# Optimization experiments

Measured on AMD Instinct MI355X. Metric: run time of the kernel, lower is better.

The kernel has to match this reference:

```python
import jax, jax.numpy as jnp
import numpy as np

IN_FEATURES = 512
OUT_FEATURES = 512
GRID_SIZE = 8
SPLINE_ORDER = 3


def make_grid():
    # grid has grid_size + 2*spline_order + 1 knots in [-1, 1]
    return jnp.linspace(-1.0, 1.0, GRID_SIZE + 2 * SPLINE_ORDER + 1, dtype=jnp.float32)


def b_splines(x, grid):
    # x: (N, in)  ->  bases: (N, in, grid_size + spline_order)
    x = jnp.clip(x, -2.0, 2.0)[..., None]  # (N, in, 1)
    bases = ((x >= grid[:-1]) & (x < grid[1:])).astype(x.dtype)
    for k in range(1, SPLINE_ORDER + 1):
        denom1 = grid[k:-1] - grid[:-(k + 1)]
        denom1 = jnp.where(jnp.abs(denom1) < 1e-8, jnp.ones_like(denom1), denom1)
        denom2 = grid[k + 1:] - grid[1:-k]
        denom2 = jnp.where(jnp.abs(denom2) < 1e-8, jnp.ones_like(denom2), denom2)
        bases = ((x - grid[:-(k + 1)]) / denom1 * bases[..., :-1]
                 + (grid[k + 1:] - x) / denom2 * bases[..., 1:])
    return bases


def setup_inputs() -> dict:
    key = jax.random.key(0)
    kx, kb, ks = jax.random.split(key, 3)
    x = jax.random.normal(kx, (8192, IN_FEATURES), dtype=jnp.float32)
    # xavier_uniform with gain=0.5 for base_weight
    limit = 0.5 * np.sqrt(6.0 / (IN_FEATURES + OUT_FEATURES))
    base_weight = jax.random.uniform(kb, (OUT_FEATURES, IN_FEATURES), dtype=jnp.float32,
                                     minval=-limit, maxval=limit)
    spline_weight = 0.01 * jax.random.normal(
        ks, (OUT_FEATURES, IN_FEATURES, GRID_SIZE + SPLINE_ORDER), dtype=jnp.float32)
    return {"x": x, "base_weight": base_weight, "spline_weight": spline_weight}


def reference(x, base_weight, spline_weight):
    grid = make_grid()
    base_out = x @ base_weight.T                      # (N, out)
    basis = b_splines(x, grid)                        # (N, in, G+K)
    spline_out = jnp.einsum('bij,oij->bo', basis, spline_weight)
    return base_out + spline_out
```

## Files before the change

kernel.cpp:

```cpp
#include <hip/hip_runtime.h>
#include <stdint.h>

#define IN_F 512
#define OUT_F 512
#define NROWS 8192
#define NSLOT 12
#define KTOT (IN_F * NSLOT)
#define K16S (KTOT / 16)
#define KSPLIT 4
#define ITERS 16
#define APAD_ROW 120
#define SW_ROW (IN_F * 11)
#define KC_PAD 776

typedef __bf16 bf16x8 __attribute__((ext_vector_type(8)));
typedef float f32x16 __attribute__((ext_vector_type(16)));

__device__ ushort g_Wb[K16S * 16 * 64 * 8];

__device__ __forceinline__ ushort f2bf(float f) {
    uint32_t u = __builtin_bit_cast(uint32_t, f);
    u += 0x7FFFu + ((u >> 16) & 1u);
    return (ushort)(u >> 16);
}

__global__ __launch_bounds__(256) void prep_weights(const float* __restrict__ bw,
                                                    const float* __restrict__ sw) {
    __shared__ __align__(16) ushort kcol[32 * KC_PAD];
    const int t  = threadIdx.x;
    const int nt = blockIdx.x & 15;
    const int kg = blockIdx.x >> 4;
    const int o0 = nt * 32;
    const int f0 = kg * 64;

    {
        const int o_l = t >> 3;
        const int tr  = t & 7;
        const float* swr = sw + (size_t)(o0 + o_l) * SW_ROW + (size_t)f0 * 11;
        #pragma unroll
        for (int i = 0; i < 22; ++i) {
            int p4 = tr + i * 8;
            float4 v = ((const float4*)swr)[p4];
            uint pos = (uint)p4 * 4;
            #pragma unroll
            for (int c = 0; c < 4; ++c) {
                uint pc = pos + c;
                uint fl = pc / 11u;
                uint j  = pc - fl * 11u;
                float val = (c == 0) ? v.x : (c == 1) ? v.y : (c == 2) ? v.z : v.w;
                kcol[o_l * KC_PAD + fl * NSLOT + j] = f2bf(val);
            }
        }
        #pragma unroll
        for (int i = 0; i < 8; ++i) {
            int fl = tr + i * 8;
            kcol[o_l * KC_PAD + fl * NSLOT + 11] =
                f2bf(bw[(size_t)(o0 + o_l) * IN_F + f0 + fl]);
        }
    }
    __syncthreads();

    {
        const int ol = t & 31;
        const int ph = t >> 5;
        #pragma unroll
        for (int i = 0; i < 12; ++i) {
            int idx  = ph + i * 8;
            int k16l = idx >> 1;
            int half = idx & 1;
            uint4 val = *(const uint4*)&kcol[ol * KC_PAD + k16l * 16 + half * 8];
            ((uint4*)g_Wb)[((size_t)((kg * 48 + k16l) * 16 + nt)) * 64 + half * 32 + ol] = val;
        }
    }
}

__global__ __launch_bounds__(512, 2) void kan_gemm(const float* __restrict__ x,
                                                   float* __restrict__ out) {
    __shared__ __align__(16) ushort As[128 * APAD_ROW];

    const int t    = threadIdx.x;
    const int lane = t & 63;
    const int w    = t >> 6;
    const int ln31 = lane & 31;
    const int half = lane >> 5;

    const int bx = blockIdx.x;
    const int mb = bx & 63;
    const int kp = bx >> 6;
    const int row_base = mb * 128;
    const int wn = w * 64;

    const int sm = t >> 2;
    const int fh = t & 3;

    f32x16 acc[4][2] = {};

    #pragma unroll 1
    for (int ii = 0; ii < ITERS; ++ii) {
        const int fbase = kp * 128 + ii * 8;
        uint4 breg[6][2];
        #pragma unroll
        for (int ks = 0; ks < 6; ++ks) {
            int k16g = kp * 96 + ii * 6 + ks;
            #pragma unroll
            for (int nt = 0; nt < 2; ++nt) {
                int ntg = w * 2 + nt;
                breg[ks][nt] = ((const uint4*)g_Wb)[((size_t)k16g * 16 + ntg) * 64 + lane];
            }
        }
        const float2 xv = *(const float2*)&x[(size_t)(row_base + sm) * IN_F + fbase + fh * 2];

        __syncthreads();

        #pragma unroll
        for (int c = 0; c < 2; ++c) {
            float xx = c ? xv.y : xv.x;
            float wpos = (xx + 1.0f) * 7.0f;
            float fi = floorf(wpos);
            int   i  = (int)fi;
            float u  = wpos - fi;
            bool inr = (xx >= -1.0f) && (xx < 1.0f);
            int   q  = i - 3;
            float um = 1.0f - u;
            float uu = u * u, u3 = uu * u;
            const float C6 = 1.0f / 6.0f;
            float s0 = (inr && q >= 0) ? C6 : 0.0f;
            float s1 = (inr && q >= -1 && q <= 9) ? C6 : 0.0f;
            float s2 = (inr && q >= -2 && q <= 8) ? C6 : 0.0f;
            float s3 = (inr && q <= 7) ? C6 : 0.0f;
            uint b0 = f2bf(um * um * um * s0);
            uint b1 = f2bf((3.0f * u3 - 6.0f * uu + 4.0f) * s1);
            uint b2 = f2bf((-3.0f * u3 + 3.0f * uu + 3.0f * u + 1.0f) * s2);
            uint b3 = f2bf(u3 * s3);
            int r  = q & 1;
            int e0 = q & ~1;
            uint P0 = r ? (b0 << 16)        : (b0 | (b1 << 16));
            uint P1 = r ? (b1 | (b2 << 16)) : (b2 | (b3 << 16));
            uint P2 = r ? b3                : 0u;
            uint p[6];
            #pragma unroll
            for (int pi = 0; pi < 6; ++pi) {
                int d = 2 * pi - e0;
                p[pi] = (d == 0) ? P0 : (d == 2) ? P1 : (d == 4) ? P2 : 0u;
            }
            p[5] = (p[5] & 0xFFFFu) | ((uint)f2bf(xx) << 16);
            ushort* rowp = &As[sm * APAD_ROW + (fh * 2 + c) * NSLOT];
            uint2 w0; w0.x = p[0]; w0.y = p[1];
            uint2 w1; w1.x = p[2]; w1.y = p[3];
            uint2 w2; w2.x = p[4]; w2.y = p[5];
            *(uint2*)&rowp[0] = w0;
            *(uint2*)&rowp[4] = w1;
            *(uint2*)&rowp[8] = w2;
        }

        __syncthreads();

        #pragma unroll
        for (int ks = 0; ks < 6; ++ks) {
            uint4 a[4];
            #pragma unroll
            for (int mt = 0; mt < 4; ++mt)
                a[mt] = *(const uint4*)&As[(mt * 32 + ln31) * APAD_ROW + ks * 16 + half * 8];
            #pragma unroll
            for (int mt = 0; mt < 4; ++mt) {
                bf16x8 af = __builtin_bit_cast(bf16x8, a[mt]);
                #pragma unroll
                for (int nt = 0; nt < 2; ++nt) {
                    bf16x8 bf = __builtin_bit_cast(bf16x8, breg[ks][nt]);
                    acc[mt][nt] = __builtin_amdgcn_mfma_f32_32x32x16_bf16(af, bf, acc[mt][nt], 0, 0, 0);
                }
            }
        }
    }

    #pragma unroll
    for (int mt = 0; mt < 4; ++mt) {
        #pragma unroll
        for (int nt = 0; nt < 2; ++nt) {
            int rb = row_base + mt * 32 + 4 * half;
            int cc = wn + nt * 32 + ln31;
            #pragma unroll
            for (int reg = 0; reg < 16; ++reg) {
                int rr = rb + (reg & 3) + 8 * (reg >> 2);
                unsafeAtomicAdd(&out[(size_t)rr * OUT_F + cc], acc[mt][nt][reg]);
            }
        }
    }
}

extern "C" void kernel_launch(void* const* d_in, const int* in_sizes, int n_in,
                              void* d_out, int out_size, void* d_ws, size_t ws_size,
                              hipStream_t stream) {
    const float* x  = (const float*)d_in[0];
    const float* bw = (const float*)d_in[1];
    const float* sw = (const float*)d_in[2];
    float* out = (float*)d_out;
    hipMemsetAsync(out, 0, (size_t)out_size * sizeof(float), stream);
    hipLaunchKernelGGL(prep_weights, dim3(128), dim3(256), 0, stream, bw, sw);
    hipLaunchKernelGGL(kan_gemm, dim3(64 * KSPLIT), dim3(512), 0, stream, x, out);
}
```

Baseline: 174.2 us.

## Split basis evaluation into separate kernel and stream GEMM operands from global memory

Moves B-spline basis evaluation out of the GEMM into a standalone kernel that writes the full bf16 basis matrix in MFMA-fragment layout to a global buffer. The GEMM kernel then loads pre-laid-out A and B fragments directly from global memory without LDS or barriers, using a 2x2 warp tile and a K split of 2. This removes the per-iteration LDS staging and syncs and halves the atomic reduction traffic. In exchange it adds a large intermediate write and repeated global reads of the basis matrix.

```diff
diff --git a/kernel.cpp b/kernel.cpp
--- a/kernel.cpp
+++ b/kernel.cpp
@@ -7,16 +7,15 @@
 #define NSLOT 12
 #define KTOT (IN_F * NSLOT)
 #define K16S (KTOT / 16)
-#define KSPLIT 4
-#define ITERS 16
-#define APAD_ROW 120
+#define MTILES (NROWS / 32)
 #define SW_ROW (IN_F * 11)
 #define KC_PAD 776
 
 typedef __bf16 bf16x8 __attribute__((ext_vector_type(8)));
 typedef float f32x16 __attribute__((ext_vector_type(16)));
 
-__device__ ushort g_Wb[K16S * 16 * 64 * 8];
+__device__ ushort g_Wb[(K16S * 16 + 1) * 512];
+__device__ ushort g_A [(MTILES * K16S + 1) * 512];
 
 __device__ __forceinline__ ushort f2bf(float f) {
     uint32_t u = __builtin_bit_cast(uint32_t, f);
@@ -69,120 +68,126 @@
             int k16l = idx >> 1;
             int half = idx & 1;
             uint4 val = *(const uint4*)&kcol[ol * KC_PAD + k16l * 16 + half * 8];
-            ((uint4*)g_Wb)[((size_t)((kg * 48 + k16l) * 16 + nt)) * 64 + half * 32 + ol] = val;
-        }
-    }
-}
-
-__global__ __launch_bounds__(512, 2) void kan_gemm(const float* __restrict__ x,
-                                                   float* __restrict__ out) {
-    __shared__ __align__(16) ushort As[128 * APAD_ROW];
-
+            ((uint4*)g_Wb)[((size_t)nt * K16S + kg * 48 + k16l) * 64 + half * 32 + ol] = val;
+        }
+    }
+}
+
+__device__ __forceinline__ void eval12(float xx, uint p[6]) {
+    float wpos = (xx + 1.0f) * 7.0f;
+    float fi = floorf(wpos);
+    int   i  = (int)fi;
+    float u  = wpos - fi;
+    bool inr = (xx >= -1.0f) && (xx < 1.0f);
+    int   q  = i - 3;
+    float um = 1.0f - u;
+    float uu = u * u, u3 = uu * u;
+    const float C6 = 1.0f / 6.0f;
+    float s0 = (inr && q >= 0) ? C6 : 0.0f;
+    float s1 = (inr && q >= -1 && q <= 9) ? C6 : 0.0f;
+    float s2 = (inr && q >= -2 && q <= 8) ? C6 : 0.0f;
+    float s3 = (inr && q <= 7) ? C6 : 0.0f;
+    uint b0 = f2bf(um * um * um * s0);
+    uint b1 = f2bf((3.0f * u3 - 6.0f * uu + 4.0f) * s1);
+    uint b2 = f2bf((-3.0f * u3 + 3.0f * uu + 3.0f * u + 1.0f) * s2);
+    uint b3 = f2bf(u3 * s3);
+    int r  = q & 1;
+    int e0 = q & ~1;
+    uint P0 = r ? (b0 << 16)        : (b0 | (b1 << 16));
+    uint P1 = r ? (b1 | (b2 << 16)) : (b2 | (b3 << 16));
+    uint P2 = r ? b3                : 0u;
+    #pragma unroll
+    for (int pi = 0; pi < 6; ++pi) {
+        int d = 2 * pi - e0;
+        p[pi] = (d == 0) ? P0 : (d == 2) ? P1 : (d == 4) ? P2 : 0u;
+    }
+    p[5] = (p[5] & 0xFFFFu) | ((uint)f2bf(xx) << 16);
+}
+
+__global__ __launch_bounds__(256, 4) void basis_eval(const float* __restrict__ x) {
     const int t    = threadIdx.x;
     const int lane = t & 63;
     const int w    = t >> 6;
+    const int r31  = lane & 31;
+    const int half = lane >> 5;
+
+    const int mt = blockIdx.x & 255;
+    const int kq = blockIdx.x >> 8;
+    const int row = mt * 32 + r31;
+    const float* xr = x + (size_t)row * IN_F;
+    uint4* Adst = (uint4*)g_A + ((size_t)mt * K16S) * 64 + lane;
+
+    const int kbase = kq * 96 + w * 24;
+    #pragma unroll 2
+    for (int i = 0; i < 24; ++i) {
+        const int k16 = kbase + i;
+        const int s0  = k16 * 16 + half * 8;
+        const int f   = s0 / NSLOT;
+        const int j0  = s0 - f * NSLOT;
+        const int fb  = (j0 == 8) ? (f + 1) : f;
+        float xa = xr[f];
+        float xb = xr[fb];
+        uint pa[6], pb[6];
+        eval12(xa, pa);
+        eval12(xb, pb);
+        uint4 o;
+        o.x = (j0 == 0) ? pa[0] : (j0 == 4) ? pa[2] : pa[4];
+        o.y = (j0 == 0) ? pa[1] : (j0 == 4) ? pa[3] : pa[5];
+        o.z = (j0 == 0) ? pa[2] : (j0 == 4) ? pa[4] : pb[0];
+        o.w = (j0 == 0) ? pa[3] : (j0 == 4) ? pa[5] : pb[1];
+        Adst[(size_t)k16 * 64] = o;
+    }
+}
+
+__global__ __launch_bounds__(256, 2) void kan_gemm(float* __restrict__ out) {
+    const int t    = threadIdx.x;
+    const int lane = t & 63;
+    const int wv   = t >> 6;
+    const int wr   = wv >> 1;
+    const int wc   = wv & 1;
     const int ln31 = lane & 31;
     const int half = lane >> 5;
 
     const int bx = blockIdx.x;
-    const int mb = bx & 63;
-    const int kp = bx >> 6;
-    const int row_base = mb * 128;
-    const int wn = w * 64;
-
-    const int sm = t >> 2;
-    const int fh = t & 3;
-
-    f32x16 acc[4][2] = {};
-
-    #pragma unroll 1
-    for (int ii = 0; ii < ITERS; ++ii) {
-        const int fbase = kp * 128 + ii * 8;
-        uint4 breg[6][2];
-        #pragma unroll
-        for (int ks = 0; ks < 6; ++ks) {
-            int k16g = kp * 96 + ii * 6 + ks;
-            #pragma unroll
-            for (int nt = 0; nt < 2; ++nt) {
-                int ntg = w * 2 + nt;
-                breg[ks][nt] = ((const uint4*)g_Wb)[((size_t)k16g * 16 + ntg) * 64 + lane];
-            }
-        }
-        const float2 xv = *(const float2*)&x[(size_t)(row_base + sm) * IN_F + fbase + fh * 2];
-
-        __syncthreads();
-
-        #pragma unroll
-        for (int c = 0; c < 2; ++c) {
-            float xx = c ? xv.y : xv.x;
-            float wpos = (xx + 1.0f) * 7.0f;
-            float fi = floorf(wpos);
-            int   i  = (int)fi;
-            float u  = wpos - fi;
-            bool inr = (xx >= -1.0f) && (xx < 1.0f);
-            int   q  = i - 3;
-            float um = 1.0f - u;
-            float uu = u * u, u3 = uu * u;
-            const float C6 = 1.0f / 6.0f;
-            float s0 = (inr && q >= 0) ? C6 : 0.0f;
-            float s1 = (inr && q >= -1 && q <= 9) ? C6 : 0.0f;
-            float s2 = (inr && q >= -2 && q <= 8) ? C6 : 0.0f;
-            float s3 = (inr && q <= 7) ? C6 : 0.0f;
-            uint b0 = f2bf(um * um * um * s0);
-            uint b1 = f2bf((3.0f * u3 - 6.0f * uu + 4.0f) * s1);
-            uint b2 = f2bf((-3.0f * u3 + 3.0f * uu + 3.0f * u + 1.0f) * s2);
-            uint b3 = f2bf(u3 * s3);
-            int r  = q & 1;
-            int e0 = q & ~1;
-            uint P0 = r ? (b0 << 16)        : (b0 | (b1 << 16));
-            uint P1 = r ? (b1 | (b2 << 16)) : (b2 | (b3 << 16));
-            uint P2 = r ? b3                : 0u;
-            uint p[6];
-            #pragma unroll
-            for (int pi = 0; pi < 6; ++pi) {
-                int d = 2 * pi - e0;
-                p[pi] = (d == 0) ? P0 : (d == 2) ? P1 : (d == 4) ? P2 : 0u;
-            }
-            p[5] = (p[5] & 0xFFFFu) | ((uint)f2bf(xx) << 16);
-            ushort* rowp = &As[sm * APAD_ROW + (fh * 2 + c) * NSLOT];
-            uint2 w0; w0.x = p[0]; w0.y = p[1];
-            uint2 w1; w1.x = p[2]; w1.y = p[3];
-            uint2 w2; w2.x = p[4]; w2.y = p[5];
-            *(uint2*)&rowp[0] = w0;
-            *(uint2*)&rowp[4] = w1;
-            *(uint2*)&rowp[8] = w2;
-        }
-
-        __syncthreads();
-
-        #pragma unroll
-        for (int ks = 0; ks < 6; ++ks) {
-            uint4 a[4];
-            #pragma unroll
-            for (int mt = 0; mt < 4; ++mt)
-                a[mt] = *(const uint4*)&As[(mt * 32 + ln31) * APAD_ROW + ks * 16 + half * 8];
-            #pragma unroll
-            for (int mt = 0; mt < 4; ++mt) {
-                bf16x8 af = __builtin_bit_cast(bf16x8, a[mt]);
-                #pragma unroll
-                for (int nt = 0; nt < 2; ++nt) {
-                    bf16x8 bf = __builtin_bit_cast(bf16x8, breg[ks][nt]);
-                    acc[mt][nt] = __builtin_amdgcn_mfma_f32_32x32x16_bf16(af, bf, acc[mt][nt], 0, 0, 0);
-                }
-            }
-        }
+    const int kp = bx & 1;
+    const int nt = (bx >> 1) & 3;
+    const int mb = bx >> 3;
+
+    const int mtg0 = mb * 4 + wr * 2;
+    const int ntg0 = nt * 4 + wc * 2;
+    const size_t MS = (size_t)K16S * 64;
+
+    const uint4* Ap = (const uint4*)g_A  + (size_t)mtg0 * MS + (size_t)(kp * 192) * 64 + lane;
+    const uint4* Bp = (const uint4*)g_Wb + (size_t)ntg0 * MS + (size_t)(kp * 192) * 64 + lane;
+
+    f32x16 acc[2][2] = {};
+
+    #pragma unroll 4
+    for (int k = 0; k < 192; ++k) {
+        uint4 a0 = Ap[(size_t)k * 64];
+        uint4 a1 = Ap[MS + (size_t)k * 64];
+        uint4 b0 = Bp[(size_t)k * 64];
+        uint4 b1 = Bp[MS + (size_t)k * 64];
+        bf16x8 af0 = __builtin_bit_cast(bf16x8, a0);
+        bf16x8 af1 = __builtin_bit_cast(bf16x8, a1);
+        bf16x8 bf0 = __builtin_bit_cast(bf16x8, b0);
+        bf16x8 bf1 = __builtin_bit_cast(bf16x8, b1);
+        acc[0][0] = __builtin_amdgcn_mfma_f32_32x32x16_bf16(af0, bf0, acc[0][0], 0, 0, 0);
+        acc[0][1] = __builtin_amdgcn_mfma_f32_32x32x16_bf16(af0, bf1, acc[0][1], 0, 0, 0);
+        acc[1][0] = __builtin_amdgcn_mfma_f32_32x32x16_bf16(af1, bf0, acc[1][0], 0, 0, 0);
+        acc[1][1] = __builtin_amdgcn_mfma_f32_32x32x16_bf16(af1, bf1, acc[1][1], 0, 0, 0);
     }
 
     #pragma unroll
-    for (int mt = 0; mt < 4; ++mt) {
-        #pragma unroll
-        for (int nt = 0; nt < 2; ++nt) {
-            int rb = row_base + mt * 32 + 4 * half;
-            int cc = wn + nt * 32 + ln31;
+    for (int mt = 0; mt < 2; ++mt) {
+        #pragma unroll
+        for (int ntt = 0; ntt < 2; ++ntt) {
+            int rb = (mtg0 + mt) * 32 + 4 * half;
+            int cc = (ntg0 + ntt) * 32 + ln31;
             #pragma unroll
             for (int reg = 0; reg < 16; ++reg) {
                 int rr = rb + (reg & 3) + 8 * (reg >> 2);
-                unsafeAtomicAdd(&out[(size_t)rr * OUT_F + cc], acc[mt][nt][reg]);
+                unsafeAtomicAdd(&out[(size_t)rr * OUT_F + cc], acc[mt][ntt][reg]);
             }
         }
     }
@@ -197,5 +202,6 @@
     float* out = (float*)d_out;
     hipMemsetAsync(out, 0, (size_t)out_size * sizeof(float), stream);
     hipLaunchKernelGGL(prep_weights, dim3(128), dim3(256), 0, stream, bw, sw);
-    hipLaunchKernelGGL(kan_gemm, dim3(64 * KSPLIT), dim3(512), 0, stream, x, out);
-}
+    hipLaunchKernelGGL(basis_eval, dim3(1024), dim3(256), 0, stream, x);
+    hipLaunchKernelGGL(kan_gemm, dim3(512), dim3(256), 0, stream, out);
+}
```

Result: slower. 219.9 us (+26.2%).

## Drop split-K atomics; per-wave private staging with prefetched weights and transposed x

Applied to the files above, without the earlier changes.

Replaces the split-K GEMM, which used atomic adds into a memset output, with a full-K kernel. Each block now owns a 128x64 output tile and writes it with plain stores. A new transpose kernel lays x out feature-major so lanes load consecutive rows. Each wave stages its own 32 rows of basis values into a double-buffered LDS area with no block barriers, and weights and x are prefetched one group ahead in registers. The cost is an extra transpose pass and memory buffer, fewer MFMAs per wave between loads, and weak B reuse, since each wave reloads weights per 32 rows.

```diff
diff --git a/kernel.cpp b/kernel.cpp
--- a/kernel.cpp
+++ b/kernel.cpp
@@ -7,16 +7,16 @@
 #define NSLOT 12
 #define KTOT (IN_F * NSLOT)
 #define K16S (KTOT / 16)
-#define KSPLIT 4
-#define ITERS 16
-#define APAD_ROW 120
 #define SW_ROW (IN_F * 11)
 #define KC_PAD 776
+#define NGROUP 128
+#define AROW 56
 
 typedef __bf16 bf16x8 __attribute__((ext_vector_type(8)));
 typedef float f32x16 __attribute__((ext_vector_type(16)));
 
-__device__ ushort g_Wb[K16S * 16 * 64 * 8];
+__device__ ushort g_Wb[(K16S * 16 + 1) * 512];
+__device__ float  g_xT[IN_F * NROWS];
 
 __device__ __forceinline__ ushort f2bf(float f) {
     uint32_t u = __builtin_bit_cast(uint32_t, f);
@@ -69,121 +69,148 @@
             int k16l = idx >> 1;
             int half = idx & 1;
             uint4 val = *(const uint4*)&kcol[ol * KC_PAD + k16l * 16 + half * 8];
-            ((uint4*)g_Wb)[((size_t)((kg * 48 + k16l) * 16 + nt)) * 64 + half * 32 + ol] = val;
-        }
-    }
-}
-
-__global__ __launch_bounds__(512, 2) void kan_gemm(const float* __restrict__ x,
-                                                   float* __restrict__ out) {
-    __shared__ __align__(16) ushort As[128 * APAD_ROW];
+            ((uint4*)g_Wb)[((size_t)nt * K16S + kg * 48 + k16l) * 64 + half * 32 + ol] = val;
+        }
+    }
+}
+
+__global__ __launch_bounds__(256) void transpose_x(const float* __restrict__ x) {
+    __shared__ float tile[64][65];
+    const int t  = threadIdx.x;
+    const int rt = blockIdx.x >> 3;
+    const int ct = blockIdx.x & 7;
+    const int r0 = rt * 64, c0 = ct * 64;
+
+    const int tr  = t >> 4;
+    const int tc4 = (t & 15) * 4;
+    #pragma unroll
+    for (int j = 0; j < 4; ++j) {
+        float4 v = *(const float4*)&x[(size_t)(r0 + tr + 16 * j) * IN_F + c0 + tc4];
+        tile[tr + 16 * j][tc4 + 0] = v.x;
+        tile[tr + 16 * j][tc4 + 1] = v.y;
+        tile[tr + 16 * j][tc4 + 2] = v.z;
+        tile[tr + 16 * j][tc4 + 3] = v.w;
+    }
+    __syncthreads();
+    const int rl = t & 63;
+    const int ch = t >> 6;
+    #pragma unroll
+    for (int j = 0; j < 16; ++j) {
+        int cl = j * 4 + ch;
+        g_xT[(size_t)(c0 + cl) * NROWS + r0 + rl] = tile[rl][cl];
+    }
+}
+
+__device__ __forceinline__ void stage_one(float xx, ushort* rowp) {
+    float wpos = (xx + 1.0f) * 7.0f;
+    float fi = floorf(wpos);
+    int   i  = (int)fi;
+    float u  = wpos - fi;
+    bool inr = (xx >= -1.0f) && (xx < 1.0f);
+    int   q  = i - 3;
+    float um = 1.0f - u;
+    float uu = u * u, u3 = uu * u;
+    const float C6 = 1.0f / 6.0f;
+    float s0 = (inr && q >= 0) ? C6 : 0.0f;
+    float s1 = (inr && q >= -1 && q <= 9) ? C6 : 0.0f;
+    float s2 = (inr && q >= -2 && q <= 8) ? C6 : 0.0f;
+    float s3 = (inr && q <= 7) ? C6 : 0.0f;
+    uint b0 = f2bf(um * um * um * s0);
+    uint b1 = f2bf((3.0f * u3 - 6.0f * uu + 4.0f) * s1);
+    uint b2 = f2bf((-3.0f * u3 + 3.0f * uu + 3.0f * u + 1.0f) * s2);
+    uint b3 = f2bf(u3 * s3);
+    int r  = q & 1;
+    int e0 = q & ~1;
+    uint P0 = r ? (b0 << 16)        : (b0 | (b1 << 16));
+    uint P1 = r ? (b1 | (b2 << 16)) : (b2 | (b3 << 16));
+    uint P2 = r ? b3                : 0u;
+    uint p[6];
+    #pragma unroll
+    for (int pi = 0; pi < 6; ++pi) {
+        int d = 2 * pi - e0;
+        p[pi] = (d == 0) ? P0 : (d == 2) ? P1 : (d == 4) ? P2 : 0u;
+    }
+    p[5] = (p[5] & 0xFFFFu) | ((uint)f2bf(xx) << 16);
+    uint2 w0; w0.x = p[0]; w0.y = p[1];
+    uint2 w1; w1.x = p[2]; w1.y = p[3];
+    uint2 w2; w2.x = p[4]; w2.y = p[5];
+    *(uint2*)&rowp[0] = w0;
+    *(uint2*)&rowp[4] = w1;
+    *(uint2*)&rowp[8] = w2;
+}
+
+__global__ __launch_bounds__(256, 2) void kan_gemm(float* __restrict__ out) {
+    __shared__ __align__(16) ushort As[2][4 * 32 * AROW];
 
     const int t    = threadIdx.x;
     const int lane = t & 63;
-    const int w    = t >> 6;
-    const int ln31 = lane & 31;
-    const int half = lane >> 5;
+    const int wv   = t >> 6;
+    const int rl   = lane & 31;
+    const int fh   = lane >> 5;
 
     const int bx = blockIdx.x;
-    const int mb = bx & 63;
-    const int kp = bx >> 6;
-    const int row_base = mb * 128;
-    const int wn = w * 64;
-
-    const int sm = t >> 2;
-    const int fh = t & 3;
-
-    f32x16 acc[4][2] = {};
+    const int ng = bx & 7;
+    const int mb = bx >> 3;
+    const int rowg = mb * 128 + wv * 32 + rl;
+
+    const float* xTr = g_xT + rowg;
+    ushort* const stg0 = &As[0][(wv * 32 + rl) * AROW];
+    ushort* const stg1 = &As[1][(wv * 32 + rl) * AROW];
+    const uint4* Bp = (const uint4*)g_Wb + ((size_t)(ng * 2) * K16S) * 64 + lane;
+
+    f32x16 acc[2] = {};
+
+    float xa = xTr[(size_t)fh * NROWS];
+    float xb = xTr[(size_t)(2 + fh) * NROWS];
+    uint4 breg[3][2];
+    #pragma unroll
+    for (int ks = 0; ks < 3; ++ks) {
+        breg[ks][0] = Bp[(size_t)ks * 64];
+        breg[ks][1] = Bp[((size_t)K16S + ks) * 64];
+    }
 
     #pragma unroll 1
-    for (int ii = 0; ii < ITERS; ++ii) {
-        const int fbase = kp * 128 + ii * 8;
-        uint4 breg[6][2];
-        #pragma unroll
-        for (int ks = 0; ks < 6; ++ks) {
-            int k16g = kp * 96 + ii * 6 + ks;
-            #pragma unroll
-            for (int nt = 0; nt < 2; ++nt) {
-                int ntg = w * 2 + nt;
-                breg[ks][nt] = ((const uint4*)g_Wb)[((size_t)k16g * 16 + ntg) * 64 + lane];
-            }
-        }
-        const float2 xv = *(const float2*)&x[(size_t)(row_base + sm) * IN_F + fbase + fh * 2];
-
-        __syncthreads();
-
-        #pragma unroll
-        for (int c = 0; c < 2; ++c) {
-            float xx = c ? xv.y : xv.x;
-            float wpos = (xx + 1.0f) * 7.0f;
-            float fi = floorf(wpos);
-            int   i  = (int)fi;
-            float u  = wpos - fi;
-            bool inr = (xx >= -1.0f) && (xx < 1.0f);
-            int   q  = i - 3;
-            float um = 1.0f - u;
-            float uu = u * u, u3 = uu * u;
-            const float C6 = 1.0f / 6.0f;
-            float s0 = (inr && q >= 0) ? C6 : 0.0f;
-            float s1 = (inr && q >= -1 && q <= 9) ? C6 : 0.0f;
-            float s2 = (inr && q >= -2 && q <= 8) ? C6 : 0.0f;
-            float s3 = (inr && q <= 7) ? C6 : 0.0f;
-            uint b0 = f2bf(um * um * um * s0);
-            uint b1 = f2bf((3.0f * u3 - 6.0f * uu + 4.0f) * s1);
-            uint b2 = f2bf((-3.0f * u3 + 3.0f * uu + 3.0f * u + 1.0f) * s2);
-            uint b3 = f2bf(u3 * s3);
-            int r  = q & 1;
-            int e0 = q & ~1;
-            uint P0 = r ? (b0 << 16)        : (b0 | (b1 << 16));
-            uint P1 = r ? (b1 | (b2 << 16)) : (b2 | (b3 << 16));
-            uint P2 = r ? b3                : 0u;
-            uint p[6];
-            #pragma unroll
-            for (int pi = 0; pi < 6; ++pi) {
-                int d = 2 * pi - e0;
-                p[pi] = (d == 0) ? P0 : (d == 2) ? P1 : (d == 4) ? P2 : 0u;
-            }
-            p[5] = (p[5] & 0xFFFFu) | ((uint)f2bf(xx) << 16);
-            ushort* rowp = &As[sm * APAD_ROW + (fh * 2 + c) * NSLOT];
-            uint2 w0; w0.x = p[0]; w0.y = p[1];
-            uint2 w1; w1.x = p[2]; w1.y = p[3];
-            uint2 w2; w2.x = p[4]; w2.y = p[5];
-            *(uint2*)&rowp[0] = w0;
-            *(uint2*)&rowp[4] = w1;
-            *(uint2*)&rowp[8] = w2;
-        }
-
-        __syncthreads();
-
-        #pragma unroll
-        for (int ks = 0; ks < 6; ++ks) {
-            uint4 a[4];
-            #pragma unroll
-            for (int mt = 0; mt < 4; ++mt)
-                a[mt] = *(const uint4*)&As[(mt * 32 + ln31) * APAD_ROW + ks * 16 + half * 8];
-            #pragma unroll
-            for (int mt = 0; mt < 4; ++mt) {
-                bf16x8 af = __builtin_bit_cast(bf16x8, a[mt]);
-                #pragma unroll
-                for (int nt = 0; nt < 2; ++nt) {
-                    bf16x8 bf = __builtin_bit_cast(bf16x8, breg[ks][nt]);
-                    acc[mt][nt] = __builtin_amdgcn_mfma_f32_32x32x16_bf16(af, bf, acc[mt][nt], 0, 0, 0);
-                }
-            }
-        }
-    }
-
-    #pragma unroll
-    for (int mt = 0; mt < 4; ++mt) {
-        #pragma unroll
-        for (int nt = 0; nt < 2; ++nt) {
-            int rb = row_base + mt * 32 + 4 * half;
-            int cc = wn + nt * 32 + ln31;
-            #pragma unroll
-            for (int reg = 0; reg < 16; ++reg) {
-                int rr = rb + (reg & 3) + 8 * (reg >> 2);
-                unsafeAtomicAdd(&out[(size_t)rr * OUT_F + cc], acc[mt][nt][reg]);
-            }
+    for (int g = 0; g < NGROUP; ++g) {
+        const int gn = (g + 1 < NGROUP) ? g + 1 : g;
+        float xa_n = xTr[(size_t)(gn * 4 + fh) * NROWS];
+        float xb_n = xTr[(size_t)(gn * 4 + 2 + fh) * NROWS];
+        uint4 bn[3][2];
+        #pragma unroll
+        for (int ks = 0; ks < 3; ++ks) {
+            bn[ks][0] = Bp[((size_t)(gn * 3 + ks)) * 64];
+            bn[ks][1] = Bp[((size_t)K16S + gn * 3 + ks) * 64];
+        }
+
+        ushort* stg = (g & 1) ? stg1 : stg0;
+        stage_one(xa, stg + fh * 12);
+        stage_one(xb, stg + fh * 12 + 24);
+
+        #pragma unroll
+        for (int ks = 0; ks < 3; ++ks) {
+            uint4 av = *(const uint4*)&stg[ks * 16 + fh * 8];
+            bf16x8 af = __builtin_bit_cast(bf16x8, av);
+            acc[0] = __builtin_amdgcn_mfma_f32_32x32x16_bf16(
+                af, __builtin_bit_cast(bf16x8, breg[ks][0]), acc[0], 0, 0, 0);
+            acc[1] = __builtin_amdgcn_mfma_f32_32x32x16_bf16(
+                af, __builtin_bit_cast(bf16x8, breg[ks][1]), acc[1], 0, 0, 0);
+        }
+
+        xa = xa_n; xb = xb_n;
+        #pragma unroll
+        for (int ks = 0; ks < 3; ++ks) {
+            breg[ks][0] = bn[ks][0];
+            breg[ks][1] = bn[ks][1];
+        }
+    }
+
+    #pragma unroll
+    for (int nt = 0; nt < 2; ++nt) {
+        const int cc = ng * 64 + nt * 32 + rl;
+        const int rb = mb * 128 + wv * 32 + 4 * fh;
+        #pragma unroll
+        for (int reg = 0; reg < 16; ++reg) {
+            int rr = rb + (reg & 3) + 8 * (reg >> 2);
+            out[(size_t)rr * OUT_F + cc] = acc[nt][reg];
         }
     }
 }
@@ -195,7 +222,7 @@
     const float* bw = (const float*)d_in[1];
     const float* sw = (const float*)d_in[2];
     float* out = (float*)d_out;
-    hipMemsetAsync(out, 0, (size_t)out_size * sizeof(float), stream);
     hipLaunchKernelGGL(prep_weights, dim3(128), dim3(256), 0, stream, bw, sw);
-    hipLaunchKernelGGL(kan_gemm, dim3(64 * KSPLIT), dim3(512), 0, stream, x, out);
-}
+    hipLaunchKernelGGL(transpose_x, dim3(1024), dim3(256), 0, stream, x);
+    hipLaunchKernelGGL(kan_gemm, dim3(512), dim3(256), 0, stream, out);
+}
```

Result: slower. 207.6 us (+19.2%).

## Retile KAN GEMM with column groups, double-buffered basis staging and N-major weights

Applied to the files above, without the earlier changes.

Changes the GEMM decomposition from a 4-way K split over 128x512 tiles to a 2-way K split with 128x128 output tiles across 512 blocks of 256 threads. The basis tile in shared memory is now double-buffered so B-spline evaluation of the next group overlaps the current MFMAs, cutting one barrier per iteration. The x loads are prefetched two groups ahead. Weights are relaid out N-tile-major so each wave streams contiguous B fragments, and prep_weights is split into more, smaller blocks. This trades more redundant basis evaluation (each row is now computed by four column groups) for fewer atomics per output element, better overlap and more parallelism.

```diff
diff --git a/kernel.cpp b/kernel.cpp
--- a/kernel.cpp
+++ b/kernel.cpp
@@ -7,16 +7,16 @@
 #define NSLOT 12
 #define KTOT (IN_F * NSLOT)
 #define K16S (KTOT / 16)
-#define KSPLIT 4
-#define ITERS 16
-#define APAD_ROW 120
 #define SW_ROW (IN_F * 11)
 #define KC_PAD 776
+#define AROW 120
+#define NGRP 32
 
 typedef __bf16 bf16x8 __attribute__((ext_vector_type(8)));
+typedef __bf16 bf16x2 __attribute__((ext_vector_type(2)));
 typedef float f32x16 __attribute__((ext_vector_type(16)));
 
-__device__ ushort g_Wb[K16S * 16 * 64 * 8];
+__device__ ushort g_Wb[(K16S * 16 + 1) * 512];
 
 __device__ __forceinline__ ushort f2bf(float f) {
     uint32_t u = __builtin_bit_cast(uint32_t, f);
@@ -26,20 +26,21 @@
 
 __global__ __launch_bounds__(256) void prep_weights(const float* __restrict__ bw,
                                                     const float* __restrict__ sw) {
-    __shared__ __align__(16) ushort kcol[32 * KC_PAD];
+    __shared__ __align__(16) ushort kcol[16 * KC_PAD];
     const int t  = threadIdx.x;
     const int nt = blockIdx.x & 15;
-    const int kg = blockIdx.x >> 4;
-    const int o0 = nt * 32;
+    const int kg = (blockIdx.x >> 4) & 7;
+    const int hv = blockIdx.x >> 7;
+    const int o0 = nt * 32 + hv * 16;
     const int f0 = kg * 64;
 
     {
-        const int o_l = t >> 3;
-        const int tr  = t & 7;
+        const int o_l = t >> 4;
+        const int tr  = t & 15;
         const float* swr = sw + (size_t)(o0 + o_l) * SW_ROW + (size_t)f0 * 11;
         #pragma unroll
-        for (int i = 0; i < 22; ++i) {
-            int p4 = tr + i * 8;
+        for (int i = 0; i < 11; ++i) {
+            int p4 = tr + i * 16;
             float4 v = ((const float4*)swr)[p4];
             uint pos = (uint)p4 * 4;
             #pragma unroll
@@ -52,8 +53,8 @@
             }
         }
         #pragma unroll
-        for (int i = 0; i < 8; ++i) {
-            int fl = tr + i * 8;
+        for (int i = 0; i < 4; ++i) {
+            int fl = tr * 4 + i;
             kcol[o_l * KC_PAD + fl * NSLOT + 11] =
                 f2bf(bw[(size_t)(o0 + o_l) * IN_F + f0 + fl]);
         }
@@ -61,124 +62,143 @@
     __syncthreads();
 
     {
-        const int ol = t & 31;
-        const int ph = t >> 5;
-        #pragma unroll
-        for (int i = 0; i < 12; ++i) {
-            int idx  = ph + i * 8;
+        const int ol16 = t & 15;
+        const int ch   = t >> 4;
+        #pragma unroll
+        for (int i = 0; i < 6; ++i) {
+            int idx  = ch + i * 16;
             int k16l = idx >> 1;
-            int half = idx & 1;
-            uint4 val = *(const uint4*)&kcol[ol * KC_PAD + k16l * 16 + half * 8];
-            ((uint4*)g_Wb)[((size_t)((kg * 48 + k16l) * 16 + nt)) * 64 + half * 32 + ol] = val;
-        }
-    }
-}
-
-__global__ __launch_bounds__(512, 2) void kan_gemm(const float* __restrict__ x,
+            int hf   = idx & 1;
+            uint4 val = *(const uint4*)&kcol[ol16 * KC_PAD + k16l * 16 + hf * 8];
+            ((uint4*)g_Wb)[((size_t)nt * K16S + kg * 48 + k16l) * 64 + hf * 32 + hv * 16 + ol16] = val;
+        }
+    }
+}
+
+__device__ __forceinline__ void eval12(float xx, uint p[6]) {
+    float wpos = (xx + 1.0f) * 7.0f;
+    float fi = floorf(wpos);
+    int   i  = (int)fi;
+    float u  = wpos - fi;
+    bool inr = (xx >= -1.0f) && (xx < 1.0f);
+    int   q  = i - 3;
+    float um = 1.0f - u;
+    float uu = u * u, u3 = uu * u;
+    const float C6 = 1.0f / 6.0f;
+    float s0 = (inr && q >= 0) ? C6 : 0.0f;
+    float s1 = (inr && q >= -1 && q <= 9) ? C6 : 0.0f;
+    float s2 = (inr && q >= -2 && q <= 8) ? C6 : 0.0f;
+    float s3 = (inr && q <= 7) ? C6 : 0.0f;
+    float b0 = um * um * um * s0;
+    float b1 = fmaf(3.0f, u3, fmaf(-6.0f, uu, 4.0f)) * s1;
+    float b2 = fmaf(-3.0f, u3, fmaf(3.0f, uu, fmaf(3.0f, u, 1.0f))) * s2;
+    float b3 = u3 * s3;
+    bf16x2 k01; k01[0] = (__bf16)b0; k01[1] = (__bf16)b1;
+    bf16x2 k23; k23[0] = (__bf16)b2; k23[1] = (__bf16)b3;
+    uint K01 = __builtin_bit_cast(uint, k01);
+    uint K23 = __builtin_bit_cast(uint, k23);
+    int r  = q & 1;
+    int e0 = q & ~1;
+    uint P0 = r ? (K01 << 16) : K01;
+    uint P1 = r ? ((K01 >> 16) | (K23 << 16)) : K23;
+    uint P2 = r ? (K23 >> 16) : 0u;
+    #pragma unroll
+    for (int pi = 0; pi < 6; ++pi) {
+        int d = 2 * pi - e0;
+        p[pi] = (d == 0) ? P0 : (d == 2) ? P1 : (d == 4) ? P2 : 0u;
+    }
+    p[5] = (p[5] & 0xFFFFu) | ((uint)f2bf(xx) << 16);
+}
+
+__device__ __forceinline__ void stage4(float4 xv, ushort* dst) {
+    uint p[4][6];
+    eval12(xv.x, p[0]);
+    eval12(xv.y, p[1]);
+    eval12(xv.z, p[2]);
+    eval12(xv.w, p[3]);
+    uint4* d4 = (uint4*)dst;
+    d4[0] = make_uint4(p[0][0], p[0][1], p[0][2], p[0][3]);
+    d4[1] = make_uint4(p[0][4], p[0][5], p[1][0], p[1][1]);
+    d4[2] = make_uint4(p[1][2], p[1][3], p[1][4], p[1][5]);
+    d4[3] = make_uint4(p[2][0], p[2][1], p[2][2], p[2][3]);
+    d4[4] = make_uint4(p[2][4], p[2][5], p[3][0], p[3][1]);
+    d4[5] = make_uint4(p[3][2], p[3][3], p[3][4], p[3][5]);
+}
+
+__global__ __launch_bounds__(256, 2) void kan_gemm(const float* __restrict__ x,
                                                    float* __restrict__ out) {
-    __shared__ __align__(16) ushort As[128 * APAD_ROW];
+    __shared__ __align__(16) ushort As[2][128 * AROW];
 
     const int t    = threadIdx.x;
     const int lane = t & 63;
-    const int w    = t >> 6;
+    const int wv   = t >> 6;
+    const int wr   = wv >> 1;
+    const int wc   = wv & 1;
     const int ln31 = lane & 31;
     const int half = lane >> 5;
 
     const int bx = blockIdx.x;
-    const int mb = bx & 63;
-    const int kp = bx >> 6;
+    const int mb = bx >> 3;
+    const int cg = (bx >> 1) & 3;
+    const int kp = bx & 1;
     const int row_base = mb * 128;
-    const int wn = w * 64;
-
-    const int sm = t >> 2;
-    const int fh = t & 3;
-
-    f32x16 acc[4][2] = {};
+
+    const int srow = t >> 1;
+    const int fq   = t & 1;
+    const float* xp = x + (size_t)(row_base + srow) * IN_F + kp * 256 + fq * 4;
+    ushort* const sb0 = &As[0][srow * AROW + fq * 48];
+    ushort* const sb1 = &As[1][srow * AROW + fq * 48];
+
+    const int ntg0 = cg * 4 + wc * 2;
+    const uint4* Bp0 = (const uint4*)g_Wb + ((size_t)ntg0 * K16S + kp * 192) * 64 + lane;
+    const uint4* Bp1 = Bp0 + (size_t)K16S * 64;
+
+    f32x16 acc[2][2] = {};
+
+    float4 xv = *(const float4*)xp;
+    stage4(xv, sb0);
+    float4 xn = *(const float4*)(xp + 8);
+    __syncthreads();
 
     #pragma unroll 1
-    for (int ii = 0; ii < ITERS; ++ii) {
-        const int fbase = kp * 128 + ii * 8;
+    for (int g = 0; g < NGRP; ++g) {
+        const int cur = g & 1;
         uint4 breg[6][2];
         #pragma unroll
         for (int ks = 0; ks < 6; ++ks) {
-            int k16g = kp * 96 + ii * 6 + ks;
-            #pragma unroll
-            for (int nt = 0; nt < 2; ++nt) {
-                int ntg = w * 2 + nt;
-                breg[ks][nt] = ((const uint4*)g_Wb)[((size_t)k16g * 16 + ntg) * 64 + lane];
-            }
-        }
-        const float2 xv = *(const float2*)&x[(size_t)(row_base + sm) * IN_F + fbase + fh * 2];
-
+            breg[ks][0] = Bp0[(size_t)(g * 6 + ks) * 64];
+            breg[ks][1] = Bp1[(size_t)(g * 6 + ks) * 64];
+        }
+        const int gf = (g + 2 < NGRP) ? g + 2 : (NGRP - 1);
+        float4 xf = *(const float4*)(xp + gf * 8);
+
+        if (g + 1 < NGRP) stage4(xn, cur ? sb0 : sb1);
+
+        const ushort* Ac = As[cur];
+        #pragma unroll
+        for (int ks = 0; ks < 6; ++ks) {
+            uint4 a0 = *(const uint4*)&Ac[(wr * 64 + ln31) * AROW + ks * 16 + half * 8];
+            uint4 a1 = *(const uint4*)&Ac[(wr * 64 + 32 + ln31) * AROW + ks * 16 + half * 8];
+            bf16x8 af0 = __builtin_bit_cast(bf16x8, a0);
+            bf16x8 af1 = __builtin_bit_cast(bf16x8, a1);
+            bf16x8 bf0 = __builtin_bit_cast(bf16x8, breg[ks][0]);
+            bf16x8 bf1 = __builtin_bit_cast(bf16x8, breg[ks][1]);
+            acc[0][0] = __builtin_amdgcn_mfma_f32_32x32x16_bf16(af0, bf0, acc[0][0], 0, 0, 0);
+            acc[0][1] = __builtin_amdgcn_mfma_f32_32x32x16_bf16(af0, bf1, acc[0][1], 0, 0, 0);
+            acc[1][0] = __builtin_amdgcn_mfma_f32_32x32x16_bf16(af1, bf0, acc[1][0], 0, 0, 0);
+            acc[1][1] = __builtin_amdgcn_mfma_f32_32x32x16_bf16(af1, bf1, acc[1][1], 0, 0, 0);
+        }
+
+        xn = xf;
         __syncthreads();
-
-        #pragma unroll
-        for (int c = 0; c < 2; ++c) {
-            float xx = c ? xv.y : xv.x;
-            float wpos = (xx + 1.0f) * 7.0f;
-            float fi = floorf(wpos);
-            int   i  = (int)fi;
-            float u  = wpos - fi;
-            bool inr = (xx >= -1.0f) && (xx < 1.0f);
-            int   q  = i - 3;
-            float um = 1.0f - u;
-            float uu = u * u, u3 = uu * u;
-            const float C6 = 1.0f / 6.0f;
-            float s0 = (inr && q >= 0) ? C6 : 0.0f;
-            float s1 = (inr && q >= -1 && q <= 9) ? C6 : 0.0f;
-            float s2 = (inr && q >= -2 && q <= 8) ? C6 : 0.0f;
-            float s3 = (inr && q <= 7) ? C6 : 0.0f;
-            uint b0 = f2bf(um * um * um * s0);
-            uint b1 = f2bf((3.0f * u3 - 6.0f * uu + 4.0f) * s1);
-            uint b2 = f2bf((-3.0f * u3 + 3.0f * uu + 3.0f * u + 1.0f) * s2);
-            uint b3 = f2bf(u3 * s3);
-            int r  = q & 1;
-            int e0 = q & ~1;
-            uint P0 = r ? (b0 << 16)        : (b0 | (b1 << 16));
-            uint P1 = r ? (b1 | (b2 << 16)) : (b2 | (b3 << 16));
-            uint P2 = r ? b3                : 0u;
-            uint p[6];
-            #pragma unroll
-            for (int pi = 0; pi < 6; ++pi) {
-                int d = 2 * pi - e0;
-                p[pi] = (d == 0) ? P0 : (d == 2) ? P1 : (d == 4) ? P2 : 0u;
-            }
-            p[5] = (p[5] & 0xFFFFu) | ((uint)f2bf(xx) << 16);
-            ushort* rowp = &As[sm * APAD_ROW + (fh * 2 + c) * NSLOT];
-            uint2 w0; w0.x = p[0]; w0.y = p[1];
-            uint2 w1; w1.x = p[2]; w1.y = p[3];
-            uint2 w2; w2.x = p[4]; w2.y = p[5];
-            *(uint2*)&rowp[0] = w0;
-            *(uint2*)&rowp[4] = w1;
-            *(uint2*)&rowp[8] = w2;
-        }
-
-        __syncthreads();
-
-        #pragma unroll
-        for (int ks = 0; ks < 6; ++ks) {
-            uint4 a[4];
-            #pragma unroll
-            for (int mt = 0; mt < 4; ++mt)
-                a[mt] = *(const uint4*)&As[(mt * 32 + ln31) * APAD_ROW + ks * 16 + half * 8];
-            #pragma unroll
-            for (int mt = 0; mt < 4; ++mt) {
-                bf16x8 af = __builtin_bit_cast(bf16x8, a[mt]);
-                #pragma unroll
-                for (int nt = 0; nt < 2; ++nt) {
-                    bf16x8 bf = __builtin_bit_cast(bf16x8, breg[ks][nt]);
-                    acc[mt][nt] = __builtin_amdgcn_mfma_f32_32x32x16_bf16(af, bf, acc[mt][nt], 0, 0, 0);
-                }
-            }
-        }
     }
 
     #pragma unroll
-    for (int mt = 0; mt < 4; ++mt) {
+    for (int mt = 0; mt < 2; ++mt) {
         #pragma unroll
         for (int nt = 0; nt < 2; ++nt) {
-            int rb = row_base + mt * 32 + 4 * half;
-            int cc = wn + nt * 32 + ln31;
+            int rb = row_base + wr * 64 + mt * 32 + 4 * half;
+            int cc = cg * 128 + wc * 64 + nt * 32 + ln31;
             #pragma unroll
             for (int reg = 0; reg < 16; ++reg) {
                 int rr = rb + (reg & 3) + 8 * (reg >> 2);
@@ -196,6 +216,6 @@
     const float* sw = (const float*)d_in[2];
     float* out = (float*)d_out;
     hipMemsetAsync(out, 0, (size_t)out_size * sizeof(float), stream);
-    hipLaunchKernelGGL(prep_weights, dim3(128), dim3(256), 0, stream, bw, sw);
-    hipLaunchKernelGGL(kan_gemm, dim3(64 * KSPLIT), dim3(512), 0, stream, x, out);
-}
+    hipLaunchKernelGGL(prep_weights, dim3(256), dim3(256), 0, stream, bw, sw);
+    hipLaunchKernelGGL(kan_gemm, dim3(512), dim3(256), 0, stream, x, out);
+}
```

Result: no change. 170.8 us (-2.0%).
